# Kernel optimization log

Hardware: AMD Instinct MI355X
Metric: run time of the kernel (lower is better)

Reference implementation:

```python
import jax, jax.numpy as jnp
import numpy as np
import math

H = 2048        # hidden_size
I = 8192        # intermediate_size
NH = 16         # num_heads
NKV = 4         # num_kv_heads
HD = 128        # head_dim
RD = 128        # rope_dim
THETA = 1000000.0
C = 8192        # context_length
EPS = 1e-6


def setup_inputs() -> dict:
    key = jax.random.key(0)
    ks = jax.random.split(key, 12)
    s = 0.02
    w = lambda k, shape: jax.random.normal(k, shape, jnp.float32) * s
    inp = {
        "hidden_states": jax.random.normal(ks[0], (1, 1, H), jnp.float32),
        "current_pos": jnp.array([4000], dtype=jnp.int32),
        "causal_mask": jnp.zeros((1, 1, 1, C), jnp.float32),
        "Wq": w(ks[1], (NH * HD * 2, H)),
        "Wk": w(ks[2], (NKV * HD, H)),
        "Wv": w(ks[3], (NKV * HD, H)),
        "Wo": w(ks[4], (H, NH * HD)),
        "q_norm": jnp.ones((HD,), jnp.float32),
        "k_norm": jnp.ones((HD,), jnp.float32),
        "ln1_w": jnp.ones((H,), jnp.float32),
        "ln2_w": jnp.ones((H,), jnp.float32),
        "W_gate": w(ks[5], (I, H)),
        "W_up": w(ks[6], (I, H)),
        "W_down": w(ks[7], (H, I)),
        "kv_cache": jax.random.normal(ks[8], (2, NKV, C, HD), jnp.float32) * 0.5,
    }
    inv_freq = 1.0 / (THETA ** (jnp.arange(0, RD, 2, dtype=jnp.float32) / RD))
    freqs = jnp.arange(C, dtype=jnp.float32)[:, None] * inv_freq[None, :]  # [C, RD/2]
    inp["rope_cos"] = jnp.cos(freqs)
    inp["rope_sin"] = jnp.sin(freqs)
    return inp


def _rms(x, w):
    return x * jax.lax.rsqrt(jnp.mean(x * x, axis=-1, keepdims=True) + EPS) * w


def _rope(x, cos, sin):
    # x: [heads, head_dim]; cos/sin: [RD/2]
    half = RD // 2
    x1, x2, xp = x[:, :half], x[:, half:RD], x[:, RD:]
    return jnp.concatenate([x1 * cos - x2 * sin, x2 * cos + x1 * sin, xp], axis=-1)


def reference(hidden_states, current_pos, causal_mask, Wq, Wk, Wv, Wo,
              q_norm, k_norm, ln1_w, ln2_w, W_gate, W_up, W_down,
              kv_cache, rope_cos, rope_sin):
    residual = hidden_states
    h = _rms(hidden_states, ln1_w)[0, 0]                  # [H]
    qg = (Wq @ h).reshape(NH, 2 * HD)
    q, gate = qg[:, :HD], qg[:, HD:]
    k = (Wk @ h).reshape(NKV, HD)
    v = (Wv @ h).reshape(NKV, HD)
    q = _rms(q, q_norm)
    k = _rms(k, k_norm)
    p = current_pos[0]
    cos, sin = rope_cos[p], rope_sin[p]
    q = _rope(q, cos, sin)
    k = _rope(k, cos, sin)
    z = jnp.int32(0)
    kc = jax.lax.dynamic_update_slice(kv_cache[0], k[:, None, :], (z, p, z))  # [NKV, C, HD]
    vc = jax.lax.dynamic_update_slice(kv_cache[1], v[:, None, :], (z, p, z))
    groups = NH // NKV
    k_exp = jnp.repeat(kc, groups, axis=0)                # [NH, C, HD]
    v_exp = jnp.repeat(vc, groups, axis=0)
    scale = 1.0 / math.sqrt(HD)
    scores = jnp.einsum('hd,hcd->hc', q, k_exp) * scale + causal_mask.reshape(1, C)
    attn = jax.nn.softmax(scores, axis=-1)
    attn_out = jnp.einsum('hc,hcd->hd', attn, v_exp) * jax.nn.sigmoid(gate)
    out = (Wo @ attn_out.reshape(NH * HD)).reshape(1, 1, H)
    x = residual + out
    h2 = _rms(x, ln2_w)
    ffn = (jax.nn.silu(h2 @ W_gate.T) * (h2 @ W_up.T)) @ W_down.T
    return x + ffn
```

## Files before the change

kernel.cpp:

```cpp
#include <hip/hip_runtime.h>

typedef unsigned short u16;
typedef unsigned int u32;

#define H 2048
#define NH 16
#define NKV 4
#define HD 128
#define CTX 8192
#define IDIM 8192
#define EPS 1e-6f
#define SCALE 0.08838834764831845f

__device__ __forceinline__ float wave_sum(float x){
#pragma unroll
    for(int o=32;o>0;o>>=1) x += __shfl_xor(x,o,64);
    return x;
}
__device__ __forceinline__ float wave_max(float x){
#pragma unroll
    for(int o=32;o>0;o>>=1) x = fmaxf(x,__shfl_xor(x,o,64));
    return x;
}

__global__ __launch_bounds__(256) void k_qkv(const float* __restrict__ Wq,
                                             const float* __restrict__ Wk,
                                             const float* __restrict__ Wv,
                                             const float* __restrict__ hs,
                                             const float* __restrict__ ln1,
                                             float* __restrict__ qg,
                                             float* __restrict__ kvec,
                                             float* __restrict__ vvec){
    __shared__ float hw[H];
    __shared__ float red[4];
    int tid = threadIdx.x, wid = tid>>6, lane = tid&63;
    float4 a = *(const float4*)(hs + tid*8);
    float4 b = *(const float4*)(hs + tid*8 + 4);
    float ss = a.x*a.x+a.y*a.y+a.z*a.z+a.w*a.w + b.x*b.x+b.y*b.y+b.z*b.z+b.w*b.w;
    ss = wave_sum(ss);
    if(lane==0) red[wid] = ss;
    __syncthreads();
    float rs = rsqrtf((red[0]+red[1]+red[2]+red[3])/(float)H + EPS);
    float4 wa = *(const float4*)(ln1 + tid*8);
    float4 wb = *(const float4*)(ln1 + tid*8 + 4);
    hw[tid*8+0]=a.x*rs*wa.x; hw[tid*8+1]=a.y*rs*wa.y;
    hw[tid*8+2]=a.z*rs*wa.z; hw[tid*8+3]=a.w*rs*wa.w;
    hw[tid*8+4]=b.x*rs*wb.x; hw[tid*8+5]=b.y*rs*wb.y;
    hw[tid*8+6]=b.z*rs*wb.z; hw[tid*8+7]=b.w*rs*wb.w;
    __syncthreads();

    int row = blockIdx.x*4 + wid;
    const float* wr; float* op;
    if(row < 4096)      { wr = Wq + (size_t)row*H;        op = qg   + row; }
    else if(row < 4608) { wr = Wk + (size_t)(row-4096)*H; op = kvec + (row-4096); }
    else                { wr = Wv + (size_t)(row-4608)*H; op = vvec + (row-4608); }
    float4 r[8];
#pragma unroll
    for(int i=0;i<8;i++) r[i] = *(const float4*)(wr + i*256 + lane*4);
    float acc = 0.f;
#pragma unroll
    for(int i=0;i<8;i++){
        const float* hp = hw + i*256 + lane*4;
        acc += r[i].x*hp[0] + r[i].y*hp[1] + r[i].z*hp[2] + r[i].w*hp[3];
    }
    acc = wave_sum(acc);
    if(lane==0) *op = acc;
}

__global__ __launch_bounds__(64) void k_rope(const float* __restrict__ qg,
                                             const float* __restrict__ kvec,
                                             const float* __restrict__ vvec,
                                             const int* __restrict__ pos,
                                             const float* __restrict__ qn,
                                             const float* __restrict__ kn,
                                             const float* __restrict__ rc,
                                             const float* __restrict__ rsn,
                                             float* __restrict__ q_rope,
                                             float* __restrict__ gate_sig,
                                             float* __restrict__ knew,
                                             float* __restrict__ vnew){
    int b = blockIdx.x, lane = threadIdx.x;
    int p = pos[0];
    float c = rc[(size_t)p*64 + lane];
    float s = rsn[(size_t)p*64 + lane];
    if(b < NH){
        int h = b;
        float x1 = qg[h*256 + lane], x2 = qg[h*256 + 64 + lane];
        float ssq = wave_sum(x1*x1 + x2*x2);
        float r = rsqrtf(ssq/128.f + EPS);
        float n1 = x1*r*qn[lane];
        float n2 = x2*r*qn[lane+64];
        q_rope[h*128 + lane]      = n1*c - n2*s;
        q_rope[h*128 + 64 + lane] = n2*c + n1*s;
        float g1 = qg[h*256 + 128 + lane], g2 = qg[h*256 + 192 + lane];
        gate_sig[h*128 + lane]      = 1.f/(1.f + __expf(-g1));
        gate_sig[h*128 + 64 + lane] = 1.f/(1.f + __expf(-g2));
    } else {
        int j = b - NH;
        float x1 = kvec[j*128 + lane], x2 = kvec[j*128 + 64 + lane];
        float ssq = wave_sum(x1*x1 + x2*x2);
        float r = rsqrtf(ssq/128.f + EPS);
        float n1 = x1*r*kn[lane];
        float n2 = x2*r*kn[lane+64];
        knew[j*128 + lane]      = n1*c - n2*s;
        knew[j*128 + 64 + lane] = n2*c + n1*s;
        vnew[j*128 + lane]      = vvec[j*128 + lane];
        vnew[j*128 + 64 + lane] = vvec[j*128 + 64 + lane];
    }
}

__global__ __launch_bounds__(128) void k_attn_part(const float* __restrict__ cache,
                                                   const float* __restrict__ q_rope,
                                                   const float* __restrict__ mask,
                                                   const int* __restrict__ pos,
                                                   const float* __restrict__ knew,
                                                   const float* __restrict__ vnew,
                                                   float* __restrict__ part_m,
                                                   float* __restrict__ part_l,
                                                   float* __restrict__ part_o,
                                                   int nchunk, int chunk){
    int j = blockIdx.y, ci = blockIdx.x, tid = threadIdx.x;
    int p = pos[0];
    __shared__ float q_s[512];
    __shared__ float s_s[512];
    __shared__ float m_s[4], l_s[4], mt_s[4], lt_s[4];
#pragma unroll
    for(int t=0;t<4;t++) q_s[t*128 + tid] = q_rope[j*512 + t*128 + tid];
    if(tid < 4){ m_s[tid] = -3.0e38f; l_s[tid] = 0.f; }
    float o0=0.f,o1=0.f,o2=0.f,o3=0.f;
    __syncthreads();
    int base0 = ci*chunk;
    for(int s0=0; s0<chunk; s0+=128){
        int c = base0 + s0 + tid;
        const float* kr = (c==p) ? (knew + (size_t)j*HD)
                                 : (cache + ((size_t)j*CTX + c)*HD);
        float a0=0.f,a1=0.f,a2=0.f,a3=0.f;
#pragma unroll
        for(int dd=0; dd<HD; dd+=4){
            float4 u = *(const float4*)(kr + dd);
            const float* q0=q_s+dd; const float* q1=q_s+128+dd;
            const float* q2=q_s+256+dd; const float* q3=q_s+384+dd;
            a0 += q0[0]*u.x+q0[1]*u.y+q0[2]*u.z+q0[3]*u.w;
            a1 += q1[0]*u.x+q1[1]*u.y+q1[2]*u.z+q1[3]*u.w;
            a2 += q2[0]*u.x+q2[1]*u.y+q2[2]*u.z+q2[3]*u.w;
            a3 += q3[0]*u.x+q3[1]*u.y+q3[2]*u.z+q3[3]*u.w;
        }
        float mv = mask[c];
        s_s[tid]       = a0*SCALE + mv;
        s_s[128 + tid] = a1*SCALE + mv;
        s_s[256 + tid] = a2*SCALE + mv;
        s_s[384 + tid] = a3*SCALE + mv;
        __syncthreads();
        int wid = tid>>6, lane = tid&63;
#pragma unroll
        for(int hh=0; hh<2; hh++){
            int h = wid*2 + hh;
            float v0 = s_s[h*128 + lane], v1 = s_s[h*128 + 64 + lane];
            float m = wave_max(fmaxf(v0, v1));
            float l = wave_sum(__expf(v0 - m) + __expf(v1 - m));
            if(lane==0){ mt_s[h]=m; lt_s[h]=l; }
        }
        __syncthreads();
        float mn[4], sc_old[4];
#pragma unroll
        for(int h=0;h<4;h++){
            mn[h] = fmaxf(m_s[h], mt_s[h]);
            sc_old[h] = __expf(m_s[h] - mn[h]);
        }
        float w0 = __expf(s_s[tid]       - mn[0]);
        float w1 = __expf(s_s[128 + tid] - mn[1]);
        float w2 = __expf(s_s[256 + tid] - mn[2]);
        float w3 = __expf(s_s[384 + tid] - mn[3]);
        __syncthreads();
        s_s[tid]=w0; s_s[128+tid]=w1; s_s[256+tid]=w2; s_s[384+tid]=w3;
        if(tid < 4){
            l_s[tid] = l_s[tid]*sc_old[tid] + lt_s[tid]*__expf(mt_s[tid] - mn[tid]);
            m_s[tid] = mn[tid];
        }
        __syncthreads();
        o0 *= sc_old[0]; o1 *= sc_old[1]; o2 *= sc_old[2]; o3 *= sc_old[3];
        const float* vb = cache + (size_t)NKV*CTX*HD + ((size_t)j*CTX + base0 + s0)*HD;
        for(int cc=0; cc<128; cc++){
            int gpos = base0 + s0 + cc;
            const float* vrow = (gpos==p) ? (vnew + (size_t)j*HD) : (vb + (size_t)cc*HD);
            float v = vrow[tid];
            o0 += s_s[cc]*v;
            o1 += s_s[128+cc]*v;
            o2 += s_s[256+cc]*v;
            o3 += s_s[384+cc]*v;
        }
        __syncthreads();
    }
    int h0 = j*4;
    part_o[((size_t)(h0+0)*nchunk + ci)*128 + tid] = o0;
    part_o[((size_t)(h0+1)*nchunk + ci)*128 + tid] = o1;
    part_o[((size_t)(h0+2)*nchunk + ci)*128 + tid] = o2;
    part_o[((size_t)(h0+3)*nchunk + ci)*128 + tid] = o3;
    if(tid < 4){
        part_m[(h0+tid)*nchunk + ci] = m_s[tid];
        part_l[(h0+tid)*nchunk + ci] = l_s[tid];
    }
}

__global__ __launch_bounds__(128) void k_attn_red(const float* __restrict__ part_m,
                                                  const float* __restrict__ part_l,
                                                  const float* __restrict__ part_o,
                                                  const float* __restrict__ gate_sig,
                                                  float* __restrict__ attn,
                                                  int nchunk){
    int h = blockIdx.x, d = threadIdx.x;
    float mg = -3.0e38f;
    for(int i=0;i<nchunk;i++) mg = fmaxf(mg, part_m[h*nchunk + i]);
    float lg = 0.f, oa = 0.f;
    for(int i=0;i<nchunk;i++){
        float e = __expf(part_m[h*nchunk + i] - mg);
        lg += part_l[h*nchunk + i]*e;
        oa += e*part_o[((size_t)h*nchunk + i)*128 + d];
    }
    attn[h*128 + d] = oa/lg * gate_sig[h*128 + d];
}

__global__ __launch_bounds__(256) void k_wo(const float* __restrict__ Wo,
                                            const float* __restrict__ attn,
                                            const float* __restrict__ resid,
                                            float* __restrict__ x){
    int wid = threadIdx.x>>6, lane = threadIdx.x&63;
    int row = blockIdx.x*4 + wid;
    const float* wr = Wo + (size_t)row*H;
    float4 r[8];
#pragma unroll
    for(int i=0;i<8;i++) r[i] = *(const float4*)(wr + i*256 + lane*4);
    float acc = 0.f;
#pragma unroll
    for(int i=0;i<8;i++){
        float4 hv = *(const float4*)(attn + i*256 + lane*4);
        acc += r[i].x*hv.x + r[i].y*hv.y + r[i].z*hv.z + r[i].w*hv.w;
    }
    acc = wave_sum(acc);
    if(lane==0) x[row] = resid[row] + acc;
}

__global__ __launch_bounds__(256) void k_rms(const float* __restrict__ in,
                                             const float* __restrict__ w,
                                             float* __restrict__ out){
    __shared__ float red[4];
    int tid = threadIdx.x;
    float4 a = *(const float4*)(in + (size_t)tid*8);
    float4 b = *(const float4*)(in + (size_t)tid*8 + 4);
    float x[8] = {a.x,a.y,a.z,a.w,b.x,b.y,b.z,b.w};
    float ss = 0.f;
#pragma unroll
    for(int i=0;i<8;i++) ss += x[i]*x[i];
    ss = wave_sum(ss);
    if((tid&63)==0) red[tid>>6] = ss;
    __syncthreads();
    float tot = red[0]+red[1]+red[2]+red[3];
    float rs = rsqrtf(tot/(float)H + EPS);
    float4 wa = *(const float4*)(w + (size_t)tid*8);
    float4 wb = *(const float4*)(w + (size_t)tid*8 + 4);
    float4 o1 = make_float4(x[0]*rs*wa.x, x[1]*rs*wa.y, x[2]*rs*wa.z, x[3]*rs*wa.w);
    float4 o2 = make_float4(x[4]*rs*wb.x, x[5]*rs*wb.y, x[6]*rs*wb.z, x[7]*rs*wb.w);
    *(float4*)(out + (size_t)tid*8)     = o1;
    *(float4*)(out + (size_t)tid*8 + 4) = o2;
}

__global__ __launch_bounds__(256) void k_gateup(const float* __restrict__ Wg,
                                                const float* __restrict__ Wu,
                                                const float* __restrict__ h2,
                                                float* __restrict__ act){
    int wid = threadIdx.x>>6, lane = threadIdx.x&63;
    int row = blockIdx.x*4 + wid;
    const float* gr = Wg + (size_t)row*H;
    const float* ur = Wu + (size_t)row*H;
    float4 g[8], u[8];
#pragma unroll
    for(int i=0;i<8;i++) g[i] = *(const float4*)(gr + i*256 + lane*4);
#pragma unroll
    for(int i=0;i<8;i++) u[i] = *(const float4*)(ur + i*256 + lane*4);
    float ag = 0.f, au = 0.f;
#pragma unroll
    for(int i=0;i<8;i++){
        float4 hv = *(const float4*)(h2 + i*256 + lane*4);
        ag += g[i].x*hv.x + g[i].y*hv.y + g[i].z*hv.z + g[i].w*hv.w;
        au += u[i].x*hv.x + u[i].y*hv.y + u[i].z*hv.z + u[i].w*hv.w;
    }
    ag = wave_sum(ag);
    au = wave_sum(au);
    if(lane==0){
        float sg = ag/(1.f + __expf(-ag));
        act[row] = sg*au;
    }
}

__global__ __launch_bounds__(256) void k_down(const float* __restrict__ Wd,
                                              const float* __restrict__ act,
                                              const float* __restrict__ x,
                                              float* __restrict__ out){
    __shared__ float part[4];
    int tid = threadIdx.x, wid = tid>>6, lane = tid&63;
    int row  = blockIdx.x*2 + (wid>>1);
    int half = wid&1;
    const float* wr = Wd + (size_t)row*IDIM + half*4096;
    float4 r[16];
#pragma unroll
    for(int i=0;i<16;i++) r[i] = *(const float4*)(wr + i*256 + lane*4);
    float acc = 0.f;
#pragma unroll
    for(int i=0;i<16;i++){
        float4 av = *(const float4*)(act + half*4096 + i*256 + lane*4);
        acc += r[i].x*av.x + r[i].y*av.y + r[i].z*av.z + r[i].w*av.w;
    }
    acc = wave_sum(acc);
    if(lane==0) part[wid] = acc;
    __syncthreads();
    if(tid < 2){
        int rr = blockIdx.x*2 + tid;
        out[rr] = x[rr] + part[tid*2] + part[tid*2+1];
    }
}

extern "C" void kernel_launch(void* const* d_in, const int* in_sizes, int n_in,
                              void* d_out, int out_size, void* d_ws, size_t ws_size,
                              hipStream_t stream){
    const float* hs   = (const float*)d_in[0];
    const int*   pos  = (const int*)d_in[1];
    const float* mask = (const float*)d_in[2];
    const float* Wq   = (const float*)d_in[3];
    const float* Wk   = (const float*)d_in[4];
    const float* Wv   = (const float*)d_in[5];
    const float* Wo   = (const float*)d_in[6];
    const float* qn   = (const float*)d_in[7];
    const float* kn   = (const float*)d_in[8];
    const float* ln1  = (const float*)d_in[9];
    const float* ln2  = (const float*)d_in[10];
    const float* Wg   = (const float*)d_in[11];
    const float* Wu   = (const float*)d_in[12];
    const float* Wd   = (const float*)d_in[13];
    const float* cache= (const float*)d_in[14];
    const float* rc   = (const float*)d_in[15];
    const float* rsn  = (const float*)d_in[16];
    float* out = (float*)d_out;

    float* ws       = (float*)d_ws;
    float* qg       = ws;
    float* kvec     = ws + 4096;
    float* vvec     = ws + 4608;
    float* q_rope   = ws + 5120;
    float* gate_sig = ws + 7168;
    float* xres     = ws + 9216;
    float* h2       = ws + 13312;
    float* attn     = ws + 15360;
    float* act      = ws + 17408;
    float* knew     = ws + 25600;
    float* vnew     = ws + 26112;
    int nchunk = 64;
    while(nchunk > 1){
        size_t need = (size_t)(26624 + 2*NH*nchunk + (size_t)NH*nchunk*128) * 4;
        if(need <= ws_size) break;
        nchunk >>= 1;
    }
    int chunk = CTX / nchunk;
    float* part_m = ws + 26624;
    float* part_l = part_m + NH*nchunk;
    float* part_o = part_l + NH*nchunk;

    k_qkv<<<1280,256,0,stream>>>(Wq, Wk, Wv, hs, ln1, qg, kvec, vvec);
    k_rope<<<20,64,0,stream>>>(qg, kvec, vvec, pos, qn, kn, rc, rsn, q_rope, gate_sig, knew, vnew);
    dim3 g3(nchunk, NKV);
    k_attn_part<<<g3,128,0,stream>>>(cache, q_rope, mask, pos, knew, vnew,
                                     part_m, part_l, part_o, nchunk, chunk);
    k_attn_red<<<16,128,0,stream>>>(part_m, part_l, part_o, gate_sig, attn, nchunk);
    k_wo<<<512,256,0,stream>>>(Wo, attn, hs, xres);
    k_rms<<<1,256,0,stream>>>(xres, ln2, h2);
    k_gateup<<<2048,256,0,stream>>>(Wg, Wu, h2, act);
    k_down<<<1024,256,0,stream>>>(Wd, act, xres, out);
}
```

Baseline: 327.3 us.

## Issue weight loads before RMSNorm, fuse ln2 into gate/up, batch attention loads

In the QKV and gate/up matvecs, the weight-row loads are now issued before the RMSNorm reduction, with a sched_barrier so HBM latency overlaps the norm. The separate single-block k_rms launch is removed; each gate/up block recomputes the ln2 RMSNorm into shared memory, saving a launch and a serial dependency at the cost of redundant per-block work. In the attention partial kernel, K and V loads are batched (8 float4 and 16 rows at a time) ahead of the FMAs to raise memory-level parallelism. Sched barriers are also added in k_wo and k_down.

```diff
diff --git a/kernel.cpp b/kernel.cpp
--- a/kernel.cpp
+++ b/kernel.cpp
@@ -1,7 +1,4 @@
 #include <hip/hip_runtime.h>
-
-typedef unsigned short u16;
-typedef unsigned int u32;
 
 #define H 2048
 #define NH 16
@@ -31,32 +28,34 @@
                                              float* __restrict__ qg,
                                              float* __restrict__ kvec,
                                              float* __restrict__ vvec){
-    __shared__ float hw[H];
+    __shared__ __align__(16) float hw[H];
     __shared__ float red[4];
     int tid = threadIdx.x, wid = tid>>6, lane = tid&63;
-    float4 a = *(const float4*)(hs + tid*8);
-    float4 b = *(const float4*)(hs + tid*8 + 4);
-    float ss = a.x*a.x+a.y*a.y+a.z*a.z+a.w*a.w + b.x*b.x+b.y*b.y+b.z*b.z+b.w*b.w;
-    ss = wave_sum(ss);
-    if(lane==0) red[wid] = ss;
-    __syncthreads();
-    float rs = rsqrtf((red[0]+red[1]+red[2]+red[3])/(float)H + EPS);
-    float4 wa = *(const float4*)(ln1 + tid*8);
-    float4 wb = *(const float4*)(ln1 + tid*8 + 4);
-    hw[tid*8+0]=a.x*rs*wa.x; hw[tid*8+1]=a.y*rs*wa.y;
-    hw[tid*8+2]=a.z*rs*wa.z; hw[tid*8+3]=a.w*rs*wa.w;
-    hw[tid*8+4]=b.x*rs*wb.x; hw[tid*8+5]=b.y*rs*wb.y;
-    hw[tid*8+6]=b.z*rs*wb.z; hw[tid*8+7]=b.w*rs*wb.w;
-    __syncthreads();
-
     int row = blockIdx.x*4 + wid;
     const float* wr; float* op;
     if(row < 4096)      { wr = Wq + (size_t)row*H;        op = qg   + row; }
     else if(row < 4608) { wr = Wk + (size_t)(row-4096)*H; op = kvec + (row-4096); }
     else                { wr = Wv + (size_t)(row-4608)*H; op = vvec + (row-4608); }
+    float4 a = *(const float4*)(hs + tid*8);
+    float4 b = *(const float4*)(hs + tid*8 + 4);
+    float4 wa = *(const float4*)(ln1 + tid*8);
+    float4 wb = *(const float4*)(ln1 + tid*8 + 4);
     float4 r[8];
 #pragma unroll
     for(int i=0;i<8;i++) r[i] = *(const float4*)(wr + i*256 + lane*4);
+    __builtin_amdgcn_sched_barrier(0);
+
+    float ss = a.x*a.x+a.y*a.y+a.z*a.z+a.w*a.w + b.x*b.x+b.y*b.y+b.z*b.z+b.w*b.w;
+    ss = wave_sum(ss);
+    if(lane==0) red[wid] = ss;
+    __syncthreads();
+    float rs = rsqrtf((red[0]+red[1]+red[2]+red[3])/(float)H + EPS);
+    hw[tid*8+0]=a.x*rs*wa.x; hw[tid*8+1]=a.y*rs*wa.y;
+    hw[tid*8+2]=a.z*rs*wa.z; hw[tid*8+3]=a.w*rs*wa.w;
+    hw[tid*8+4]=b.x*rs*wb.x; hw[tid*8+5]=b.y*rs*wb.y;
+    hw[tid*8+6]=b.z*rs*wb.z; hw[tid*8+7]=b.w*rs*wb.w;
+    __syncthreads();
+
     float acc = 0.f;
 #pragma unroll
     for(int i=0;i<8;i++){
@@ -135,15 +134,21 @@
         const float* kr = (c==p) ? (knew + (size_t)j*HD)
                                  : (cache + ((size_t)j*CTX + c)*HD);
         float a0=0.f,a1=0.f,a2=0.f,a3=0.f;
-#pragma unroll
-        for(int dd=0; dd<HD; dd+=4){
-            float4 u = *(const float4*)(kr + dd);
-            const float* q0=q_s+dd; const float* q1=q_s+128+dd;
-            const float* q2=q_s+256+dd; const float* q3=q_s+384+dd;
-            a0 += q0[0]*u.x+q0[1]*u.y+q0[2]*u.z+q0[3]*u.w;
-            a1 += q1[0]*u.x+q1[1]*u.y+q1[2]*u.z+q1[3]*u.w;
-            a2 += q2[0]*u.x+q2[1]*u.y+q2[2]*u.z+q2[3]*u.w;
-            a3 += q3[0]*u.x+q3[1]*u.y+q3[2]*u.z+q3[3]*u.w;
+        for(int d0=0; d0<HD; d0+=32){
+            float4 u8[8];
+#pragma unroll
+            for(int t=0;t<8;t++) u8[t] = *(const float4*)(kr + d0 + t*4);
+            __builtin_amdgcn_sched_barrier(0);
+#pragma unroll
+            for(int t=0;t<8;t++){
+                int dd = d0 + t*4;
+                const float* q0=q_s+dd; const float* q1=q_s+128+dd;
+                const float* q2=q_s+256+dd; const float* q3=q_s+384+dd;
+                a0 += q0[0]*u8[t].x+q0[1]*u8[t].y+q0[2]*u8[t].z+q0[3]*u8[t].w;
+                a1 += q1[0]*u8[t].x+q1[1]*u8[t].y+q1[2]*u8[t].z+q1[3]*u8[t].w;
+                a2 += q2[0]*u8[t].x+q2[1]*u8[t].y+q2[2]*u8[t].z+q2[3]*u8[t].w;
+                a3 += q3[0]*u8[t].x+q3[1]*u8[t].y+q3[2]*u8[t].z+q3[3]*u8[t].w;
+            }
         }
         float mv = mask[c];
         s_s[tid]       = a0*SCALE + mv;
@@ -180,14 +185,24 @@
         __syncthreads();
         o0 *= sc_old[0]; o1 *= sc_old[1]; o2 *= sc_old[2]; o3 *= sc_old[3];
         const float* vb = cache + (size_t)NKV*CTX*HD + ((size_t)j*CTX + base0 + s0)*HD;
-        for(int cc=0; cc<128; cc++){
-            int gpos = base0 + s0 + cc;
-            const float* vrow = (gpos==p) ? (vnew + (size_t)j*HD) : (vb + (size_t)cc*HD);
-            float v = vrow[tid];
-            o0 += s_s[cc]*v;
-            o1 += s_s[128+cc]*v;
-            o2 += s_s[256+cc]*v;
-            o3 += s_s[384+cc]*v;
+        for(int cc0=0; cc0<128; cc0+=16){
+            float v[16];
+#pragma unroll
+            for(int t=0;t<16;t++){
+                int gpos = base0 + s0 + cc0 + t;
+                const float* vrow = (gpos==p) ? (vnew + (size_t)j*HD)
+                                              : (vb + (size_t)(cc0+t)*HD);
+                v[t] = vrow[tid];
+            }
+            __builtin_amdgcn_sched_barrier(0);
+#pragma unroll
+            for(int t=0;t<16;t++){
+                int cc = cc0 + t;
+                o0 += s_s[cc]*v[t];
+                o1 += s_s[128+cc]*v[t];
+                o2 += s_s[256+cc]*v[t];
+                o3 += s_s[384+cc]*v[t];
+            }
         }
         __syncthreads();
     }
@@ -230,6 +245,7 @@
     float4 r[8];
 #pragma unroll
     for(int i=0;i<8;i++) r[i] = *(const float4*)(wr + i*256 + lane*4);
+    __builtin_amdgcn_sched_barrier(0);
     float acc = 0.f;
 #pragma unroll
     for(int i=0;i<8;i++){
@@ -240,49 +256,49 @@
     if(lane==0) x[row] = resid[row] + acc;
 }
 
-__global__ __launch_bounds__(256) void k_rms(const float* __restrict__ in,
-                                             const float* __restrict__ w,
-                                             float* __restrict__ out){
-    __shared__ float red[4];
-    int tid = threadIdx.x;
-    float4 a = *(const float4*)(in + (size_t)tid*8);
-    float4 b = *(const float4*)(in + (size_t)tid*8 + 4);
-    float x[8] = {a.x,a.y,a.z,a.w,b.x,b.y,b.z,b.w};
-    float ss = 0.f;
-#pragma unroll
-    for(int i=0;i<8;i++) ss += x[i]*x[i];
-    ss = wave_sum(ss);
-    if((tid&63)==0) red[tid>>6] = ss;
-    __syncthreads();
-    float tot = red[0]+red[1]+red[2]+red[3];
-    float rs = rsqrtf(tot/(float)H + EPS);
-    float4 wa = *(const float4*)(w + (size_t)tid*8);
-    float4 wb = *(const float4*)(w + (size_t)tid*8 + 4);
-    float4 o1 = make_float4(x[0]*rs*wa.x, x[1]*rs*wa.y, x[2]*rs*wa.z, x[3]*rs*wa.w);
-    float4 o2 = make_float4(x[4]*rs*wb.x, x[5]*rs*wb.y, x[6]*rs*wb.z, x[7]*rs*wb.w);
-    *(float4*)(out + (size_t)tid*8)     = o1;
-    *(float4*)(out + (size_t)tid*8 + 4) = o2;
-}
-
 __global__ __launch_bounds__(256) void k_gateup(const float* __restrict__ Wg,
                                                 const float* __restrict__ Wu,
-                                                const float* __restrict__ h2,
+                                                const float* __restrict__ xres,
+                                                const float* __restrict__ ln2,
                                                 float* __restrict__ act){
-    int wid = threadIdx.x>>6, lane = threadIdx.x&63;
+    __shared__ __align__(16) float hw[H];
+    __shared__ float red[4];
+    int tid = threadIdx.x, wid = tid>>6, lane = tid&63;
     int row = blockIdx.x*4 + wid;
     const float* gr = Wg + (size_t)row*H;
     const float* ur = Wu + (size_t)row*H;
+    float4 a = *(const float4*)(xres + (size_t)tid*8);
+    float4 b = *(const float4*)(xres + (size_t)tid*8 + 4);
+    float4 wa = *(const float4*)(ln2 + (size_t)tid*8);
+    float4 wb = *(const float4*)(ln2 + (size_t)tid*8 + 4);
     float4 g[8], u[8];
 #pragma unroll
     for(int i=0;i<8;i++) g[i] = *(const float4*)(gr + i*256 + lane*4);
 #pragma unroll
     for(int i=0;i<8;i++) u[i] = *(const float4*)(ur + i*256 + lane*4);
+    __builtin_amdgcn_sched_barrier(0);
+
+    float x[8] = {a.x,a.y,a.z,a.w,b.x,b.y,b.z,b.w};
+    float ss = 0.f;
+#pragma unroll
+    for(int i=0;i<8;i++) ss += x[i]*x[i];
+    ss = wave_sum(ss);
+    if(lane==0) red[wid] = ss;
+    __syncthreads();
+    float tot = red[0]+red[1]+red[2]+red[3];
+    float rs = rsqrtf(tot/(float)H + EPS);
+    hw[tid*8+0]=x[0]*rs*wa.x; hw[tid*8+1]=x[1]*rs*wa.y;
+    hw[tid*8+2]=x[2]*rs*wa.z; hw[tid*8+3]=x[3]*rs*wa.w;
+    hw[tid*8+4]=x[4]*rs*wb.x; hw[tid*8+5]=x[5]*rs*wb.y;
+    hw[tid*8+6]=x[6]*rs*wb.z; hw[tid*8+7]=x[7]*rs*wb.w;
+    __syncthreads();
+
     float ag = 0.f, au = 0.f;
 #pragma unroll
     for(int i=0;i<8;i++){
-        float4 hv = *(const float4*)(h2 + i*256 + lane*4);
-        ag += g[i].x*hv.x + g[i].y*hv.y + g[i].z*hv.z + g[i].w*hv.w;
-        au += u[i].x*hv.x + u[i].y*hv.y + u[i].z*hv.z + u[i].w*hv.w;
+        const float* hp = hw + i*256 + lane*4;
+        ag += g[i].x*hp[0] + g[i].y*hp[1] + g[i].z*hp[2] + g[i].w*hp[3];
+        au += u[i].x*hp[0] + u[i].y*hp[1] + u[i].z*hp[2] + u[i].w*hp[3];
     }
     ag = wave_sum(ag);
     au = wave_sum(au);
@@ -304,6 +320,7 @@
     float4 r[16];
 #pragma unroll
     for(int i=0;i<16;i++) r[i] = *(const float4*)(wr + i*256 + lane*4);
+    __builtin_amdgcn_sched_barrier(0);
     float acc = 0.f;
 #pragma unroll
     for(int i=0;i<16;i++){
@@ -348,7 +365,6 @@
     float* q_rope   = ws + 5120;
     float* gate_sig = ws + 7168;
     float* xres     = ws + 9216;
-    float* h2       = ws + 13312;
     float* attn     = ws + 15360;
     float* act      = ws + 17408;
     float* knew     = ws + 25600;
@@ -371,7 +387,6 @@
                                      part_m, part_l, part_o, nchunk, chunk);
     k_attn_red<<<16,128,0,stream>>>(part_m, part_l, part_o, gate_sig, attn, nchunk);
     k_wo<<<512,256,0,stream>>>(Wo, attn, hs, xres);
-    k_rms<<<1,256,0,stream>>>(xres, ln2, h2);
-    k_gateup<<<2048,256,0,stream>>>(Wg, Wu, h2, act);
+    k_gateup<<<2048,256,0,stream>>>(Wg, Wu, xres, ln2, act);
     k_down<<<1024,256,0,stream>>>(Wd, act, xres, out);
 }
```

Measured after the change: 320.0 us. 2.2% less time.
